# Kernel tuning notes

Measured on AMD Instinct MI355X. Metric: run time of the kernel, lower is better.

Reference implementation:

```python
import jax, jax.numpy as jnp
import numpy as np

N = 96                      # n_size: neurons per row/column
WAVELENGTH = 1.55e-6        # telecom wavelength (m)
PITCH = 1.55e-6             # neuron spacing = wavelength (m)
Z_SRC = 0.0                 # z of this layer
Z_NEXT = 1e-5               # z of next layer


def setup_inputs() -> dict:
    key = jax.random.key(0)
    k1, k2 = jax.random.split(key)
    x = jax.random.normal(k1, (N, N), dtype=jnp.float32)
    weights = jax.random.normal(k2, (N, N), dtype=jnp.float32)
    coords = (jnp.arange(N, dtype=jnp.float32) - (N - 1) / 2.0) * PITCH
    return {"x": x, "weights": weights, "x_coords": coords, "y_coords": coords}


def reference(x, weights, x_coords, y_coords):
    # Transmission matrix: unit-amplitude, phase = weights  ->  e^{j*w}
    # (weights mod 2*pi gives the same complex value, so exp(1j*w) is exact)
    modes = (jnp.exp(1j * weights) * x).reshape(-1)          # (M,) complex64, M = N*N

    # Neuron grid positions (same x/y grid on both planes, differing only in z)
    xx, yy = jnp.meshgrid(x_coords, y_coords, indexing="ij")
    px = xx.reshape(-1)                                       # (M,)
    py = yy.reshape(-1)                                       # (M,)
    dz = Z_NEXT - Z_SRC

    # Pairwise source->detector distances, (M, M)
    dx = px[:, None] - px[None, :]
    dy = py[:, None] - py[None, :]
    r = jnp.sqrt(dx * dx + dy * dy + dz * dz)

    # First Rayleigh-Sommerfeld diffraction kernel:
    #   w(r) = (dz / r^2) * (1/(2*pi*r) + 1/(j*lambda)) * exp(j*2*pi*r/lambda) * dA
    k = 2.0 * jnp.pi / WAVELENGTH
    g = (dz / (r * r)) * (1.0 / (2.0 * jnp.pi * r) + 1.0 / (1j * WAVELENGTH)) \
        * jnp.exp(1j * k * r)                                 # (M, M) complex64

    dA = PITCH * PITCH
    out = jnp.einsum("i,ij->j", modes, g) * dA                # (M,)
    return out.reshape(N, N)
```

## Files before the change

kernel.cpp:

```cpp
#include <hip/hip_runtime.h>
#include <math.h>


#define NN 96
#define M (NN*NN)
#define GH 191
#define GW 192

__device__ float2 g_G[GH * GW];
__device__ float2 g_modes[M];

__global__ __launch_bounds__(256) void precompute_kernel(
    const float* __restrict__ x, const float* __restrict__ w,
    const float* __restrict__ xc, const float* __restrict__ yc) {
  const double DZ     = 1e-5;
  const double LAMBDA = 1.55e-6;
  const double PI     = 3.14159265358979323846;
  const double K      = 2.0 * PI / LAMBDA;
  const double DA     = 1.55e-6 * 1.55e-6;

  int idx = blockIdx.x * 256 + threadIdx.x;
  if (idx < GH * GH) {
    int u = idx / GH - (NN - 1);
    int v = idx % GH - (NN - 1);
    int au = u < 0 ? -u : u;
    int av = v < 0 ? -v : v;
    double dx = (double)xc[au] - (double)xc[0];
    double dy = (double)yc[av] - (double)yc[0];
    double r2 = dx * dx + dy * dy + DZ * DZ;
    double r  = sqrt(r2);
    double amp = DZ / r2 * DA;
    double A = amp / (2.0 * PI * r);
    double B = amp / LAMBDA;
    double s, c;
    sincos(K * r, &s, &c);
    g_G[(u + NN - 1) * GW + (v + NN - 1)] =
        make_float2((float)(A * c + B * s), (float)(A * s - B * c));
  } else if (idx < GH * GH + M) {
    int i = idx - GH * GH;
    double s, c;
    sincos((double)w[i], &s, &c);
    double xv = (double)x[i];
    g_modes[i] = make_float2((float)(c * xv), (float)(s * xv));
  }
}

__global__ __launch_bounds__(192) void conv_kernel(float* __restrict__ out,
                                                   int interleaved) {
  int c  = blockIdx.x;
  int a0 = blockIdx.y * 12;
  int t  = threadIdx.x;

  __shared__ float2 s_modes[12 * NN];
  __shared__ float2 s_G[12 * GW];
  __shared__ float2 s_red[NN];

  #pragma unroll
  for (int k = 0; k < 6; ++k)
    s_modes[k * 192 + t] = g_modes[a0 * NN + k * 192 + t];
  #pragma unroll
  for (int k = 0; k < 12; ++k)
    s_G[k * GW + t] = g_G[(a0 + k - c + (NN - 1)) * GW + t];
  __syncthreads();

  int d = t % NN;
  int h = t / NN;
  float re = 0.f, im = 0.f;
  for (int ai = h; ai < 12; ai += 2) {
    const float2* __restrict__ mrow = s_modes + ai * NN;
    const float2* __restrict__ grow = s_G + ai * GW + (NN - 1 - d);
    #pragma unroll 8
    for (int b = 0; b < NN; ++b) {
      float2 m  = mrow[b];
      float2 gv = grow[b];
      re = fmaf(m.x, gv.x, re);
      re = fmaf(-m.y, gv.y, re);
      im = fmaf(m.x, gv.y, im);
      im = fmaf(m.y, gv.x, im);
    }
  }

  if (h == 1) s_red[d] = make_float2(re, im);
  __syncthreads();
  if (h == 0) {
    re += s_red[d].x;
    im += s_red[d].y;
    int j = c * NN + d;
    if (interleaved) {
      atomicAdd(out + 2 * j,     re);
      atomicAdd(out + 2 * j + 1, im);
    } else {
      atomicAdd(out + j, re);
    }
  }
}

extern "C" void kernel_launch(void* const* d_in, const int* in_sizes, int n_in,
                              void* d_out, int out_size, void* d_ws, size_t ws_size,
                              hipStream_t stream) {
  const float* x  = (const float*)d_in[0];
  const float* w  = (const float*)d_in[1];
  const float* xc = (const float*)d_in[2];
  const float* yc = (const float*)d_in[3];
  float* out = (float*)d_out;

  hipMemsetAsync(d_out, 0, (size_t)out_size * sizeof(float), stream);

  int total = GH * GH + M;
  precompute_kernel<<<(total + 255) / 256, 256, 0, stream>>>(x, w, xc, yc);

  int interleaved = (out_size >= 2 * M) ? 1 : 0;
  conv_kernel<<<dim3(NN, 8), 192, 0, stream>>>(out, interleaved);
}
```

Before: 81.76 us.

## Register-block conv kernel over four outputs per thread with float4 LDS loads

Each thread in the convolution kernel now computes four adjacent output columns and keeps a sliding window of G values in registers, so every loaded mode is reused across four outputs and LDS traffic goes through float4 loads. The a-row tile per block shrinks from 12 to 8 and the grid grows to 12 blocks in y. All 8 row-partials are reduced through shared memory before the atomics. Mode precompute switches from double to float sincos, which lowers precision slightly.

```diff
diff --git a/kernel.cpp b/kernel.cpp
--- a/kernel.cpp
+++ b/kernel.cpp
@@ -5,9 +5,11 @@
 #define NN 96
 #define M (NN*NN)
 #define GH 191
-#define GW 192
+#define GWG 192
+#define GW2 200
+#define MW2 104
 
-__device__ float2 g_G[GH * GW];
+__device__ float2 g_G[GH * GWG];
 __device__ float2 g_modes[M];
 
 __global__ __launch_bounds__(256) void precompute_kernel(
@@ -34,58 +36,97 @@
     double B = amp / LAMBDA;
     double s, c;
     sincos(K * r, &s, &c);
-    g_G[(u + NN - 1) * GW + (v + NN - 1)] =
+    g_G[(u + NN - 1) * GWG + (v + NN - 1)] =
         make_float2((float)(A * c + B * s), (float)(A * s - B * c));
   } else if (idx < GH * GH + M) {
     int i = idx - GH * GH;
-    double s, c;
-    sincos((double)w[i], &s, &c);
-    double xv = (double)x[i];
-    g_modes[i] = make_float2((float)(c * xv), (float)(s * xv));
+    float s, c;
+    __sincosf(0.0f, &s, &c);
+    sincosf(w[i], &s, &c);
+    float xv = x[i];
+    g_modes[i] = make_float2(c * xv, s * xv);
   }
 }
 
 __global__ __launch_bounds__(192) void conv_kernel(float* __restrict__ out,
                                                    int interleaved) {
   int c  = blockIdx.x;
-  int a0 = blockIdx.y * 12;
+  int a0 = blockIdx.y * 8;
   int t  = threadIdx.x;
 
-  __shared__ float2 s_modes[12 * NN];
-  __shared__ float2 s_G[12 * GW];
-  __shared__ float2 s_red[NN];
+  __shared__ float2 s_modes[8 * MW2];
+  __shared__ float2 s_G[8 * GW2 + 8];
+  __shared__ float2 s_red[8 * NN];
 
+  {
+    float4* dst = (float4*)s_modes;
+    const float4* src = (const float4*)(g_modes + a0 * NN);
+    #pragma unroll
+    for (int k = 0; k < 2; ++k) {
+      int idx = k * 192 + t;
+      int row = idx / 48, col = idx % 48;
+      ((float4*)(s_modes + row * MW2))[col] = src[row * 48 + col];
+      (void)dst;
+    }
+  }
   #pragma unroll
-  for (int k = 0; k < 6; ++k)
-    s_modes[k * 192 + t] = g_modes[a0 * NN + k * 192 + t];
-  #pragma unroll
-  for (int k = 0; k < 12; ++k)
-    s_G[k * GW + t] = g_G[(a0 + k - c + (NN - 1)) * GW + t];
+  for (int k = 0; k < 4; ++k) {
+    int idx = k * 192 + t;
+    int row = idx / 96, col = idx % 96;
+    const float4* src = (const float4*)(g_G + (a0 + row - c + (NN - 1)) * GWG);
+    ((float4*)(s_G + row * GW2))[col] = src[col];
+  }
   __syncthreads();
 
-  int d = t % NN;
-  int h = t / NN;
-  float re = 0.f, im = 0.f;
-  for (int ai = h; ai < 12; ai += 2) {
-    const float2* __restrict__ mrow = s_modes + ai * NN;
-    const float2* __restrict__ grow = s_G + ai * GW + (NN - 1 - d);
-    #pragma unroll 8
-    for (int b = 0; b < NN; ++b) {
-      float2 m  = mrow[b];
-      float2 gv = grow[b];
-      re = fmaf(m.x, gv.x, re);
-      re = fmaf(-m.y, gv.y, re);
-      im = fmaf(m.x, gv.y, im);
-      im = fmaf(m.y, gv.x, im);
+  int q = t % 24;
+  int h = t / 24;
+  int base = 92 - 4 * q;
+  const float4* Grow = (const float4*)(s_G + h * GW2);
+  const float4* Mrow = (const float4*)(s_modes + h * MW2);
+  int gb = base >> 1;
+
+  float4 g0 = Grow[gb];
+  float4 g1 = Grow[gb + 1];
+  float4 g2 = Grow[gb + 2];
+  float2 a0c = {0.f, 0.f}, a1c = {0.f, 0.f}, a2c = {0.f, 0.f}, a3c = {0.f, 0.f};
+
+#define CFMA(acc, mr, mi, gr, gi)                 \
+  acc.x = fmaf(mr, gr, acc.x);                    \
+  acc.x = fmaf(-(mi), gi, acc.x);                 \
+  acc.y = fmaf(mr, gi, acc.y);                    \
+  acc.y = fmaf(mi, gr, acc.y)
+
+  for (int b = 0; b < NN; b += 2) {
+    float4 mm = Mrow[b >> 1];
+    CFMA(a0c, mm.x, mm.y, g1.z, g1.w);
+    CFMA(a0c, mm.z, mm.w, g2.x, g2.y);
+    CFMA(a1c, mm.x, mm.y, g1.x, g1.y);
+    CFMA(a1c, mm.z, mm.w, g1.z, g1.w);
+    CFMA(a2c, mm.x, mm.y, g0.z, g0.w);
+    CFMA(a2c, mm.z, mm.w, g1.x, g1.y);
+    CFMA(a3c, mm.x, mm.y, g0.x, g0.y);
+    CFMA(a3c, mm.z, mm.w, g0.z, g0.w);
+    g0 = g1;
+    g1 = g2;
+    g2 = Grow[gb + 3 + (b >> 1)];
+  }
+#undef CFMA
+
+  int dbase = 4 * q;
+  s_red[h * NN + dbase + 0] = a0c;
+  s_red[h * NN + dbase + 1] = a1c;
+  s_red[h * NN + dbase + 2] = a2c;
+  s_red[h * NN + dbase + 3] = a3c;
+  __syncthreads();
+
+  if (t < NN) {
+    float re = 0.f, im = 0.f;
+    #pragma unroll
+    for (int hh = 0; hh < 8; ++hh) {
+      re += s_red[hh * NN + t].x;
+      im += s_red[hh * NN + t].y;
     }
-  }
-
-  if (h == 1) s_red[d] = make_float2(re, im);
-  __syncthreads();
-  if (h == 0) {
-    re += s_red[d].x;
-    im += s_red[d].y;
-    int j = c * NN + d;
+    int j = c * NN + t;
     if (interleaved) {
       atomicAdd(out + 2 * j,     re);
       atomicAdd(out + 2 * j + 1, im);
@@ -110,5 +151,5 @@
   precompute_kernel<<<(total + 255) / 256, 256, 0, stream>>>(x, w, xc, yc);
 
   int interleaved = (out_size >= 2 * M) ? 1 : 0;
-  conv_kernel<<<dim3(NN, 8), 192, 0, stream>>>(out, interleaved);
+  conv_kernel<<<dim3(NN, 12), 192, 0, stream>>>(out, interleaved);
 }
```

After: 76.83 us. 6.0% less time.
